# Performance work log

Hardware: AMD Instinct MI355X
Metric: run time of the kernel (lower is better)

## Reference

```python
import jax, jax.numpy as jnp
import numpy as np

B, N, E, T = 32768, 6, 6, 2  # batch graphs, nodes, edges (ring), edge types
H, DIN = 128, 3


def _ring_rel():
    # off_diag[i, (i+1)%N] = 1 -> edge e: sender i, receiver (i+1)%N
    send = np.arange(N)
    recv = (np.arange(N) + 1) % N
    eye = np.eye(N, dtype=np.float32)
    return jnp.asarray(eye[recv]), jnp.asarray(eye[send])  # rel_rec, rel_send [E,N]


def setup_inputs() -> dict:
    key = jax.random.key(0)
    ks = iter(jax.random.split(key, 40))
    rn = lambda shape, s=0.1: jax.random.normal(next(ks), shape, jnp.float32) * s
    rel_rec, rel_send = _ring_rel()
    inp = {
        'x': rn((B, N, DIN), 1.0),
        'rel_rec': rel_rec, 'rel_send': rel_send,
        'e1w1': rn((DIN, H)), 'e1b1': jnp.full((H,), 0.1), 'e1w2': rn((H, H)), 'e1b2': jnp.full((H,), 0.1),
        'e2w1': rn((2 * H, H)), 'e2b1': jnp.full((H,), 0.1), 'e2w2': rn((H, H)), 'e2b2': jnp.full((H,), 0.1),
        'e3w1': rn((H, H)), 'e3b1': jnp.full((H,), 0.1), 'e3w2': rn((H, H)), 'e3b2': jnp.full((H,), 0.1),
        'e4w1': rn((2 * H, H)), 'e4b1': jnp.full((H,), 0.1), 'e4w2': rn((H, H)), 'e4b2': jnp.full((H,), 0.1),
        'ew_out': rn((H, T)), 'eb_out': jnp.full((T,), 0.1),
        'd_msg_w1': rn((T, 2 * DIN, H)), 'd_msg_b1': rn((T, H), 0.01),
        'd_msg_w2': rn((T, H, H)), 'd_msg_b2': rn((T, H), 0.01),
        'd_out_w1': rn((DIN + H, H)), 'd_out_b1': rn((H,), 0.01),
        'd_out_w2': rn((H, H)), 'd_out_b2': rn((H,), 0.01),
        'd_out_w3': rn((H, DIN)), 'd_out_b3': rn((DIN,), 0.01),
    }
    return inp


def _mlp(h, w1, b1, w2, b2):
    # two-layer ELU MLP (dropout inactive at eval)
    return jax.nn.elu(jax.nn.elu(h @ w1 + b1) @ w2 + b2)


def reference(x, rel_rec, rel_send,
              e1w1, e1b1, e1w2, e1b2, e2w1, e2b1, e2w2, e2b2,
              e3w1, e3b1, e3w2, e3b2, e4w1, e4b1, e4w2, e4b2,
              ew_out, eb_out,
              d_msg_w1, d_msg_b1, d_msg_w2, d_msg_b2,
              d_out_w1, d_out_b1, d_out_w2, d_out_b2, d_out_w3, d_out_b3):
    node2edge = lambda h: jnp.concatenate(
        [jnp.einsum('en,bnh->beh', rel_rec, h), jnp.einsum('en,bnh->beh', rel_send, h)], axis=-1)

    # ---- GraphEncoder (factor=False) ----
    h = _mlp(x, e1w1, e1b1, e1w2, e1b2)                      # [B,N,H]
    he = _mlp(node2edge(h), e2w1, e2b1, e2w2, e2b2)          # [B,E,H]
    h2 = _mlp(he, e3w1, e3b1, e3w2, e3b2)                    # [B,E,H]
    h3 = _mlp(jnp.concatenate([h2, he], -1), e4w1, e4b1, e4w2, e4b2)
    logits = h3 @ ew_out + eb_out                            # [B,E,T]
    rel_type = jax.nn.softmax(logits, axis=-1)               # edge-type weights

    # ---- GraphDecoder single step (skip_first=False) ----
    recv = jnp.einsum('en,bnd->bed', rel_rec, x)             # [B,E,DIN]
    send = jnp.einsum('en,bnd->bed', rel_send, x)
    pre_msg = jnp.concatenate([recv, send], axis=-1)         # [B,E,2*DIN]
    # batched per-edge-type MLP: one grouped GEMM instead of a python loop of layers
    m = jax.nn.relu(jnp.einsum('bei,tih->bteh', pre_msg, d_msg_w1) + d_msg_b1[None, :, None, :])
    m = jax.nn.relu(jnp.einsum('bteh,tho->bteo', m, d_msg_w2) + d_msg_b2[None, :, None, :])
    all_msgs = jnp.einsum('bteh,bet->beh', m, rel_type)      # weight + accumulate over types
    agg_msgs = jnp.einsum('beh,en->bnh', all_msgs, rel_rec)  # edge -> node aggregation

    aug = jnp.concatenate([x, agg_msgs], axis=-1)            # [B,N,DIN+H]
    p = jax.nn.relu(aug @ d_out_w1 + d_out_b1)
    p = jax.nn.relu(p @ d_out_w2 + d_out_b2)
    p = p @ d_out_w3 + d_out_b3
    return x + p                                             # [B,N,DIN]
```

## Files before the change

### kernel.cpp

```cpp
#include <hip/hip_runtime.h>
#include <hip/hip_bf16.h>

typedef __bf16 bf16x8 __attribute__((ext_vector_type(8)));
typedef float floatx4 __attribute__((ext_vector_type(4)));

#define LDW 136
#define PXW 40

#define O_E1W2  0
#define O_E2W1  16384
#define O_E2W2  49152
#define O_E3W1  65536
#define O_E3W2  81920
#define O_E4W1  98304
#define O_E4W2  131072
#define O_DM2T0 147456
#define O_DM2T1 163840
#define O_DO1   180224
#define O_DO2   196608
#define O_EWOUT 212992
#define O_DW3   215040
#define O_E1W1P 217088
#define O_M1T0P 221184
#define O_M1T1P 225280
#define O_DO1XP 229376
#define WS_ELEMS 233472

__global__ void prep_kernel(const float* e1w2, const float* e2w1, const float* e2w2,
    const float* e3w1, const float* e3w2, const float* e4w1, const float* e4w2,
    const float* dmsg2, const float* dout1, const float* dout2,
    const float* ew_out, const float* dout_w3, const float* e1w1,
    const float* dmsg_w1, __hip_bfloat16* ws) {
  int idx = blockIdx.x * 256 + threadIdx.x;
  if (idx >= WS_ELEMS) return;
  float v;
  if (idx < O_E2W1)      { int l = idx;           v = e1w2[(l & 127) * 128 + (l >> 7)]; }
  else if (idx < O_E2W2) { int l = idx - O_E2W1;  v = e2w1[(l & 255) * 128 + (l >> 8)]; }
  else if (idx < O_E3W1) { int l = idx - O_E2W2;  v = e2w2[(l & 127) * 128 + (l >> 7)]; }
  else if (idx < O_E3W2) { int l = idx - O_E3W1;  v = e3w1[(l & 127) * 128 + (l >> 7)]; }
  else if (idx < O_E4W1) { int l = idx - O_E3W2;  v = e3w2[(l & 127) * 128 + (l >> 7)]; }
  else if (idx < O_E4W2) { int l = idx - O_E4W1;  v = e4w1[(l & 255) * 128 + (l >> 8)]; }
  else if (idx < O_DM2T0){ int l = idx - O_E4W2;  v = e4w2[(l & 127) * 128 + (l >> 7)]; }
  else if (idx < O_DM2T1){ int l = idx - O_DM2T0; v = dmsg2[(l & 127) * 128 + (l >> 7)]; }
  else if (idx < O_DO1)  { int l = idx - O_DM2T1; v = dmsg2[16384 + (l & 127) * 128 + (l >> 7)]; }
  else if (idx < O_DO2)  { int l = idx - O_DO1;   v = dout1[384 + (l & 127) * 128 + (l >> 7)]; }
  else if (idx < O_EWOUT){ int l = idx - O_DO2;   v = dout2[(l & 127) * 128 + (l >> 7)]; }
  else if (idx < O_DW3)  { int l = idx - O_EWOUT; int n = l >> 7;
                           v = (n < 2) ? ew_out[(l & 127) * 2 + n] : 0.f; }
  else if (idx < O_E1W1P){ int l = idx - O_DW3;   int n = l >> 7;
                           v = (n < 3) ? dout_w3[(l & 127) * 3 + n] : 0.f; }
  else if (idx < O_M1T0P){ int l = idx - O_E1W1P; int n = l >> 5, c = l & 31;
                           v = (c >= 3 && c < 6) ? e1w1[(c - 3) * 128 + n] : 0.f; }
  else if (idx < O_M1T1P){ int l = idx - O_M1T0P; int n = l >> 5, c = l & 31;
                           v = (c < 6) ? dmsg_w1[c * 128 + n] : 0.f; }
  else if (idx < O_DO1XP){ int l = idx - O_M1T1P; int n = l >> 5, c = l & 31;
                           v = (c < 6) ? dmsg_w1[768 + c * 128 + n] : 0.f; }
  else                   { int l = idx - O_DO1XP; int n = l >> 5, c = l & 31;
                           v = (c >= 3 && c < 6) ? dout1[(c - 3) * 128 + n] : 0.f; }
  ws[idx] = __float2bfloat16(v);
}

struct W4 { bf16x8 b[4]; };
struct W8 { bf16x8 b[8]; };

__global__ __launch_bounds__(512, 4) void nri_fused(
    const float* __restrict__ x,
    const float* __restrict__ e1b1, const float* __restrict__ e1b2,
    const float* __restrict__ e2b1, const float* __restrict__ e2b2,
    const float* __restrict__ e3b1, const float* __restrict__ e3b2,
    const float* __restrict__ e4b1, const float* __restrict__ e4b2,
    const float* __restrict__ eb_out,
    const float* __restrict__ dmsg_b1, const float* __restrict__ dmsg_b2,
    const float* __restrict__ dout_b1, const float* __restrict__ dout_b2,
    const float* __restrict__ dout_b3,
    const __bf16* __restrict__ wt, float* __restrict__ out)
{
  const int tid  = threadIdx.x;
  const int wave = tid >> 6;
  const int lane = tid & 63;
  const int nl   = lane & 15;
  const int quad = lane >> 4;
  const int colb = wave * 16 + nl;
  const int gx   = blockIdx.x * 288;

  __shared__ __align__(16) __hip_bfloat16 bufA[96 * LDW];
  __shared__ __align__(16) __hip_bfloat16 bufB[96 * LDW];
  __shared__ __align__(16) __hip_bfloat16 pxb[96 * PXW];
  __shared__ __align__(16) float biasL[16 * 128];
  __shared__ float rtw[192];
  __shared__ float xs[288];
  __shared__ float obuf[288];

  for (int i = tid; i < 288; i += 512) xs[i] = x[gx + i];
  for (int i = tid; i < 2048; i += 512) {
    int row = i >> 7, c = i & 127;
    float v;
    switch (row) {
      case 0: v = e1b1[c]; break;   case 1: v = e1b2[c]; break;
      case 2: v = e2b1[c]; break;   case 3: v = e2b2[c]; break;
      case 4: v = e3b1[c]; break;   case 5: v = e3b2[c]; break;
      case 6: v = e4b1[c]; break;   case 7: v = e4b2[c]; break;
      case 8: v = dmsg_b1[c]; break;  case 9: v = dmsg_b1[128 + c]; break;
      case 10: v = dmsg_b2[c]; break; case 11: v = dmsg_b2[128 + c]; break;
      case 12: v = dout_b1[c]; break; case 13: v = dout_b2[c]; break;
      case 14: v = (c < 2) ? eb_out[c] : 0.f; break;
      default: v = (c < 3) ? dout_b3[c] : 0.f; break;
    }
    biasL[i] = v;
  }
  for (int i = tid; i < 96 * 32; i += 512) {
    int row = i >> 5, c = i & 31;
    int e = row % 6;
    float v = 0.f;
    if (c < 3)      { int rr = row + ((e == 5) ? -5 : 1); v = x[gx + rr * 3 + c]; }
    else if (c < 6) v = x[gx + row * 3 + (c - 3)];
    pxb[row * PXW + c] = __float2bfloat16(v);
  }
  __syncthreads();

  auto initb = [&](floatx4 (&a)[6], int brow) {
    float bv = biasL[brow * 128 + colb];
    floatx4 v = {bv, bv, bv, bv};
#pragma unroll
    for (int mt = 0; mt < 6; ++mt) a[mt] = v;
  };

  auto loadW128 = [&](int wofs) {
    W4 w;
    const __bf16* p = wt + wofs + colb * 128 + quad * 8;
#pragma unroll
    for (int ks = 0; ks < 4; ++ks) w.b[ks] = *(const bf16x8*)(p + ks * 32);
    return w;
  };
  auto loadW256 = [&](int wofs) {
    W8 w;
    const __bf16* p = wt + wofs + colb * 256 + quad * 8;
#pragma unroll
    for (int ks = 0; ks < 8; ++ks) w.b[ks] = *(const bf16x8*)(p + ks * 32);
    return w;
  };
  auto loadW256half = [&](int wofs, int kh) {
    W4 w;
    const __bf16* p = wt + wofs + colb * 256 + kh * 128 + quad * 8;
#pragma unroll
    for (int ks = 0; ks < 4; ++ks) w.b[ks] = *(const bf16x8*)(p + ks * 32);
    return w;
  };

  auto gemmP = [&](floatx4 (&acc)[6], const W4& w, const __hip_bfloat16* in) {
    const __bf16* ab = (const __bf16*)(const void*)in;
#pragma unroll
    for (int ks = 0; ks < 4; ++ks) {
      int kk = ks * 32 + quad * 8;
#pragma unroll
      for (int mt = 0; mt < 6; ++mt) {
        bf16x8 a = *(const bf16x8*)(ab + (mt * 16 + nl) * LDW + kk);
        acc[mt] = __builtin_amdgcn_mfma_f32_16x16x32_bf16(a, w.b[ks], acc[mt], 0, 0, 0);
      }
    }
  };
  auto gemmP2 = [&](floatx4 (&accA)[6], const W4& wA, floatx4 (&accB)[6],
                    const W4& wB, const __hip_bfloat16* in) {
    const __bf16* ab = (const __bf16*)(const void*)in;
#pragma unroll
    for (int ks = 0; ks < 4; ++ks) {
      int kk = ks * 32 + quad * 8;
#pragma unroll
      for (int mt = 0; mt < 6; ++mt) {
        bf16x8 a = *(const bf16x8*)(ab + (mt * 16 + nl) * LDW + kk);
        accA[mt] = __builtin_amdgcn_mfma_f32_16x16x32_bf16(a, wA.b[ks], accA[mt], 0, 0, 0);
        accB[mt] = __builtin_amdgcn_mfma_f32_16x16x32_bf16(a, wB.b[ks], accB[mt], 0, 0, 0);
      }
    }
  };
  auto gemm256P = [&](floatx4 (&acc)[6], const W8& w, const __hip_bfloat16* in) {
    int rofs0[6], rofs1[6];
#pragma unroll
    for (int mt = 0; mt < 6; ++mt) {
      int r = mt * 16 + nl;
      rofs1[mt] = r * LDW;
      int e = r % 6;
      rofs0[mt] = (r + ((e == 5) ? -5 : 1)) * LDW;
    }
    const __bf16* ab = (const __bf16*)(const void*)in;
#pragma unroll
    for (int ks = 0; ks < 8; ++ks) {
      int kk = (ks & 3) * 32 + quad * 8;
      const int* rofs = (ks < 4) ? rofs0 : rofs1;
#pragma unroll
      for (int mt = 0; mt < 6; ++mt) {
        bf16x8 a = *(const bf16x8*)(ab + rofs[mt] + kk);
        acc[mt] = __builtin_amdgcn_mfma_f32_16x16x32_bf16(a, w.b[ks], acc[mt], 0, 0, 0);
      }
    }
  };
  auto gemm32 = [&](floatx4 (&acc)[6], int wofs) {
    const __bf16* pb = (const __bf16*)(const void*)pxb;
    bf16x8 b0 = *(const bf16x8*)(wt + wofs + colb * 32 + quad * 8);
#pragma unroll
    for (int mt = 0; mt < 6; ++mt) {
      bf16x8 a = *(const bf16x8*)(pb + (mt * 16 + nl) * PXW + quad * 8);
      acc[mt] = __builtin_amdgcn_mfma_f32_16x16x32_bf16(a, b0, acc[mt], 0, 0, 0);
    }
  };
  auto store_act = [&](floatx4 (&acc)[6], int act, __hip_bfloat16* ob) {
#pragma unroll
    for (int mt = 0; mt < 6; ++mt)
#pragma unroll
      for (int r = 0; r < 4; ++r) {
        float z = acc[mt][r];
        if (act == 1) z = (z > 0.f) ? z : (__expf(z) - 1.f);
        else z = fmaxf(z, 0.f);
        ob[(mt * 16 + quad * 4 + r) * LDW + colb] = __float2bfloat16(z);
      }
  };

  floatx4 acc[6], acc2[6];

  initb(acc, 0); gemm32(acc, O_E1W1P);
  W4 w2 = loadW128(O_E1W2);
  store_act(acc, 1, bufA);
  __syncthreads();
  initb(acc, 1); gemmP(acc, w2, bufA);
  W8 w3 = loadW256(O_E2W1);
  store_act(acc, 1, bufB);
  __syncthreads();
  initb(acc, 2); gemm256P(acc, w3, bufB);
  W4 w4 = loadW128(O_E2W2);
  store_act(acc, 1, bufA);
  __syncthreads();
  initb(acc, 3); gemmP(acc, w4, bufA);
  W4 w5 = loadW128(O_E3W1);
  W4 w5b = loadW256half(O_E4W1, 1);
  store_act(acc, 1, bufB);
  __syncthreads();
  initb(acc, 4); initb(acc2, 6);
  gemmP2(acc, w5, acc2, w5b, bufB);
  W4 w6 = loadW128(O_E3W2);
  store_act(acc, 1, bufA);
  __syncthreads();
  initb(acc, 5); gemmP(acc, w6, bufA);
  W4 w7 = loadW256half(O_E4W1, 0);
  store_act(acc, 1, bufB);
  __syncthreads();
  gemmP(acc2, w7, bufB);
  W4 w8 = loadW128(O_E4W2);
  store_act(acc2, 1, bufA);
  __syncthreads();
  initb(acc, 7); gemmP(acc, w8, bufA);
  store_act(acc, 1, bufB);
  __syncthreads();

  if (wave < 6) {
    int tile = wave;
    float bv = biasL[14 * 128 + nl];
    floatx4 lg = {bv, bv, bv, bv};
    const __bf16* ab = (const __bf16*)(const void*)bufB;
    const __bf16* wp = wt + O_EWOUT + nl * 128 + quad * 8;
#pragma unroll
    for (int ks = 0; ks < 4; ++ks) {
      bf16x8 a = *(const bf16x8*)(ab + (tile * 16 + nl) * LDW + ks * 32 + quad * 8);
      bf16x8 b = *(const bf16x8*)(wp + ks * 32);
      lg = __builtin_amdgcn_mfma_f32_16x16x32_bf16(a, b, lg, 0, 0, 0);
    }
    if (nl < 2) {
#pragma unroll
      for (int r = 0; r < 4; ++r)
        rtw[(tile * 16 + quad * 4 + r) * 2 + nl] = lg[r];
    }
  }
  __syncthreads();

  if (tid < 96) {
    float l0 = rtw[tid * 2], l1 = rtw[tid * 2 + 1];
    float mx = fmaxf(l0, l1);
    float ea = __expf(l0 - mx), eb = __expf(l1 - mx);
    float inv = 1.f / (ea + eb);
    rtw[tid * 2] = ea * inv; rtw[tid * 2 + 1] = eb * inv;
  }
  initb(acc, 8);  gemm32(acc, O_M1T0P);  store_act(acc, 2, bufA);
  initb(acc2, 9); gemm32(acc2, O_M1T1P); store_act(acc2, 2, bufB);
  W4 wm0 = loadW128(O_DM2T0);
  W4 wm1 = loadW128(O_DM2T1);
  __syncthreads();

  initb(acc, 10);  gemmP(acc, wm0, bufA);
  initb(acc2, 11); gemmP(acc2, wm1, bufB);
#pragma unroll
  for (int mt = 0; mt < 6; ++mt)
#pragma unroll
    for (int r = 0; r < 4; ++r) {
      int row = mt * 16 + quad * 4 + r;
      float r0 = rtw[row * 2], r1 = rtw[row * 2 + 1];
      acc[mt][r] = r0 * fmaxf(acc[mt][r], 0.f) + r1 * fmaxf(acc2[mt][r], 0.f);
    }
  W4 wd1 = loadW128(O_DO1);
  __syncthreads();

#pragma unroll
  for (int mt = 0; mt < 6; ++mt)
#pragma unroll
    for (int r = 0; r < 4; ++r) {
      int row = mt * 16 + quad * 4 + r;
      int e = row % 6;
      int orow = row + ((e == 5) ? -5 : 1);
      bufA[orow * LDW + colb] = __float2bfloat16(acc[mt][r]);
    }
  __syncthreads();

  initb(acc, 12); gemmP(acc, wd1, bufA); gemm32(acc, O_DO1XP);
  W4 wd2 = loadW128(O_DO2);
  store_act(acc, 2, bufB);
  __syncthreads();
  initb(acc, 13); gemmP(acc, wd2, bufB);
  store_act(acc, 2, bufA);
  __syncthreads();

  if (wave < 6) {
    int tile = wave;
    float bv = biasL[15 * 128 + nl];
    floatx4 d = {bv, bv, bv, bv};
    const __bf16* ab = (const __bf16*)(const void*)bufA;
    const __bf16* wp = wt + O_DW3 + nl * 128 + quad * 8;
#pragma unroll
    for (int ks = 0; ks < 4; ++ks) {
      bf16x8 a = *(const bf16x8*)(ab + (tile * 16 + nl) * LDW + ks * 32 + quad * 8);
      bf16x8 b = *(const bf16x8*)(wp + ks * 32);
      d = __builtin_amdgcn_mfma_f32_16x16x32_bf16(a, b, d, 0, 0, 0);
    }
    if (nl < 3) {
#pragma unroll
      for (int r = 0; r < 4; ++r) {
        int row = tile * 16 + quad * 4 + r;
        obuf[row * 3 + nl] = xs[row * 3 + nl] + d[r];
      }
    }
  }
  __syncthreads();
  for (int i = tid; i < 288; i += 512) out[gx + i] = obuf[i];
}

extern "C" void kernel_launch(void* const* d_in, const int* in_sizes, int n_in,
                              void* d_out, int out_size, void* d_ws, size_t ws_size,
                              hipStream_t stream) {
  const float* x       = (const float*)d_in[0];
  const float* e1w1    = (const float*)d_in[3];
  const float* e1b1    = (const float*)d_in[4];
  const float* e1w2    = (const float*)d_in[5];
  const float* e1b2    = (const float*)d_in[6];
  const float* e2w1    = (const float*)d_in[7];
  const float* e2b1    = (const float*)d_in[8];
  const float* e2w2    = (const float*)d_in[9];
  const float* e2b2    = (const float*)d_in[10];
  const float* e3w1    = (const float*)d_in[11];
  const float* e3b1    = (const float*)d_in[12];
  const float* e3w2    = (const float*)d_in[13];
  const float* e3b2    = (const float*)d_in[14];
  const float* e4w1    = (const float*)d_in[15];
  const float* e4b1    = (const float*)d_in[16];
  const float* e4w2    = (const float*)d_in[17];
  const float* e4b2    = (const float*)d_in[18];
  const float* ew_out  = (const float*)d_in[19];
  const float* eb_out  = (const float*)d_in[20];
  const float* dmsg_w1 = (const float*)d_in[21];
  const float* dmsg_b1 = (const float*)d_in[22];
  const float* dmsg_w2 = (const float*)d_in[23];
  const float* dmsg_b2 = (const float*)d_in[24];
  const float* dout_w1 = (const float*)d_in[25];
  const float* dout_b1 = (const float*)d_in[26];
  const float* dout_w2 = (const float*)d_in[27];
  const float* dout_b2 = (const float*)d_in[28];
  const float* dout_w3 = (const float*)d_in[29];
  const float* dout_b3 = (const float*)d_in[30];

  prep_kernel<<<(WS_ELEMS + 255) / 256, 256, 0, stream>>>(
      e1w2, e2w1, e2w2, e3w1, e3w2, e4w1, e4w2, dmsg_w2, dout_w1, dout_w2,
      ew_out, dout_w3, e1w1, dmsg_w1, (__hip_bfloat16*)d_ws);

  nri_fused<<<32768 / 16, 512, 0, stream>>>(
      x, e1b1, e1b2, e2b1, e2b2, e3b1, e3b2, e4b1, e4b2, eb_out,
      dmsg_b1, dmsg_b2, dout_b1, dout_b2, dout_b3,
      (const __bf16*)d_ws, (float*)d_out);
}
```

Before: 267.1 us.

## Shrink LDS footprint and raise occupancy by loading biases straight to registers

Removes the shared-memory bias table, the x staging buffer and the output staging buffer. Biases and the small K=32 weight fragments are now prefetched from global memory into registers just ahead of each layer. The padded input buffer shrinks from 40 to 8 columns, and only quad 0 loads A, with the other lanes feeding zeros. Launch bounds move from 4 to 6 blocks per SM to use the freed LDS for occupancy, at the cost of tighter register limits that may cause spills. Output is written directly from the final MFMA lanes rather than through a coalesced staging pass.

```diff
diff --git a/kernel.cpp b/kernel.cpp
--- a/kernel.cpp
+++ b/kernel.cpp
@@ -5,7 +5,7 @@
 typedef float floatx4 __attribute__((ext_vector_type(4)));
 
 #define LDW 136
-#define PXW 40
+#define PXW 8
 
 #define O_E1W2  0
 #define O_E2W1  16384
@@ -63,7 +63,7 @@
 struct W4 { bf16x8 b[4]; };
 struct W8 { bf16x8 b[8]; };
 
-__global__ __launch_bounds__(512, 4) void nri_fused(
+__global__ __launch_bounds__(512, 6) void nri_fused(
     const float* __restrict__ x,
     const float* __restrict__ e1b1, const float* __restrict__ e1b2,
     const float* __restrict__ e2b1, const float* __restrict__ e2b2,
@@ -86,40 +86,22 @@
   __shared__ __align__(16) __hip_bfloat16 bufA[96 * LDW];
   __shared__ __align__(16) __hip_bfloat16 bufB[96 * LDW];
   __shared__ __align__(16) __hip_bfloat16 pxb[96 * PXW];
-  __shared__ __align__(16) float biasL[16 * 128];
   __shared__ float rtw[192];
-  __shared__ float xs[288];
-  __shared__ float obuf[288];
-
-  for (int i = tid; i < 288; i += 512) xs[i] = x[gx + i];
-  for (int i = tid; i < 2048; i += 512) {
-    int row = i >> 7, c = i & 127;
-    float v;
-    switch (row) {
-      case 0: v = e1b1[c]; break;   case 1: v = e1b2[c]; break;
-      case 2: v = e2b1[c]; break;   case 3: v = e2b2[c]; break;
-      case 4: v = e3b1[c]; break;   case 5: v = e3b2[c]; break;
-      case 6: v = e4b1[c]; break;   case 7: v = e4b2[c]; break;
-      case 8: v = dmsg_b1[c]; break;  case 9: v = dmsg_b1[128 + c]; break;
-      case 10: v = dmsg_b2[c]; break; case 11: v = dmsg_b2[128 + c]; break;
-      case 12: v = dout_b1[c]; break; case 13: v = dout_b2[c]; break;
-      case 14: v = (c < 2) ? eb_out[c] : 0.f; break;
-      default: v = (c < 3) ? dout_b3[c] : 0.f; break;
-    }
-    biasL[i] = v;
-  }
-  for (int i = tid; i < 96 * 32; i += 512) {
-    int row = i >> 5, c = i & 31;
+
+  float b_s1 = e1b1[colb];
+  bf16x8 wk_s1 = *(const bf16x8*)(wt + O_E1W1P + colb * 32 + quad * 8);
+
+  for (int i = tid; i < 96 * PXW; i += 512) {
+    int row = i >> 3, c = i & 7;
     int e = row % 6;
     float v = 0.f;
     if (c < 3)      { int rr = row + ((e == 5) ? -5 : 1); v = x[gx + rr * 3 + c]; }
     else if (c < 6) v = x[gx + row * 3 + (c - 3)];
-    pxb[row * PXW + c] = __float2bfloat16(v);
+    pxb[i] = __float2bfloat16(v);
   }
   __syncthreads();
 
-  auto initb = [&](floatx4 (&a)[6], int brow) {
-    float bv = biasL[brow * 128 + colb];
+  auto initv = [&](floatx4 (&a)[6], float bv) {
     floatx4 v = {bv, bv, bv, bv};
 #pragma unroll
     for (int mt = 0; mt < 6; ++mt) a[mt] = v;
@@ -194,13 +176,13 @@
       }
     }
   };
-  auto gemm32 = [&](floatx4 (&acc)[6], int wofs) {
+  auto gemm32 = [&](floatx4 (&acc)[6], bf16x8 wfrag) {
     const __bf16* pb = (const __bf16*)(const void*)pxb;
-    bf16x8 b0 = *(const bf16x8*)(wt + wofs + colb * 32 + quad * 8);
 #pragma unroll
     for (int mt = 0; mt < 6; ++mt) {
-      bf16x8 a = *(const bf16x8*)(pb + (mt * 16 + nl) * PXW + quad * 8);
-      acc[mt] = __builtin_amdgcn_mfma_f32_16x16x32_bf16(a, b0, acc[mt], 0, 0, 0);
+      bf16x8 a = {0, 0, 0, 0, 0, 0, 0, 0};
+      if (quad == 0) a = *(const bf16x8*)(pb + (mt * 16 + nl) * PXW);
+      acc[mt] = __builtin_amdgcn_mfma_f32_16x16x32_bf16(a, wfrag, acc[mt], 0, 0, 0);
     }
   };
   auto store_act = [&](floatx4 (&acc)[6], int act, __hip_bfloat16* ob) {
@@ -217,44 +199,55 @@
 
   floatx4 acc[6], acc2[6];
 
-  initb(acc, 0); gemm32(acc, O_E1W1P);
+  initv(acc, b_s1); gemm32(acc, wk_s1);
   W4 w2 = loadW128(O_E1W2);
+  float b_s2 = e1b2[colb];
   store_act(acc, 1, bufA);
   __syncthreads();
-  initb(acc, 1); gemmP(acc, w2, bufA);
+  initv(acc, b_s2); gemmP(acc, w2, bufA);
   W8 w3 = loadW256(O_E2W1);
+  float b_s3 = e2b1[colb];
   store_act(acc, 1, bufB);
   __syncthreads();
-  initb(acc, 2); gemm256P(acc, w3, bufB);
+  initv(acc, b_s3); gemm256P(acc, w3, bufB);
   W4 w4 = loadW128(O_E2W2);
+  float b_s4 = e2b2[colb];
   store_act(acc, 1, bufA);
   __syncthreads();
-  initb(acc, 3); gemmP(acc, w4, bufA);
+  initv(acc, b_s4); gemmP(acc, w4, bufA);
   W4 w5 = loadW128(O_E3W1);
   W4 w5b = loadW256half(O_E4W1, 1);
+  float b_s5 = e3b1[colb];
+  float b2_s5 = e4b1[colb];
   store_act(acc, 1, bufB);
   __syncthreads();
-  initb(acc, 4); initb(acc2, 6);
+  initv(acc, b_s5); initv(acc2, b2_s5);
   gemmP2(acc, w5, acc2, w5b, bufB);
   W4 w6 = loadW128(O_E3W2);
+  float b_s6 = e3b2[colb];
   store_act(acc, 1, bufA);
   __syncthreads();
-  initb(acc, 5); gemmP(acc, w6, bufA);
+  initv(acc, b_s6); gemmP(acc, w6, bufA);
   W4 w7 = loadW256half(O_E4W1, 0);
   store_act(acc, 1, bufB);
   __syncthreads();
   gemmP(acc2, w7, bufB);
   W4 w8 = loadW128(O_E4W2);
+  float b_s8 = e4b2[colb];
   store_act(acc2, 1, bufA);
   __syncthreads();
-  initb(acc, 7); gemmP(acc, w8, bufA);
+  initv(acc, b_s8); gemmP(acc, w8, bufA);
+  float ebv = (nl < 2) ? eb_out[nl] : 0.f;
+  bf16x8 wk10a = *(const bf16x8*)(wt + O_M1T0P + colb * 32 + quad * 8);
+  bf16x8 wk10b = *(const bf16x8*)(wt + O_M1T1P + colb * 32 + quad * 8);
+  float b_m0 = dmsg_b1[colb];
+  float b_m1 = dmsg_b1[128 + colb];
   store_act(acc, 1, bufB);
   __syncthreads();
 
   if (wave < 6) {
     int tile = wave;
-    float bv = biasL[14 * 128 + nl];
-    floatx4 lg = {bv, bv, bv, bv};
+    floatx4 lg = {ebv, ebv, ebv, ebv};
     const __bf16* ab = (const __bf16*)(const void*)bufB;
     const __bf16* wp = wt + O_EWOUT + nl * 128 + quad * 8;
 #pragma unroll
@@ -278,14 +271,16 @@
     float inv = 1.f / (ea + eb);
     rtw[tid * 2] = ea * inv; rtw[tid * 2 + 1] = eb * inv;
   }
-  initb(acc, 8);  gemm32(acc, O_M1T0P);  store_act(acc, 2, bufA);
-  initb(acc2, 9); gemm32(acc2, O_M1T1P); store_act(acc2, 2, bufB);
+  initv(acc, b_m0);  gemm32(acc, wk10a);  store_act(acc, 2, bufA);
+  initv(acc2, b_m1); gemm32(acc2, wk10b); store_act(acc2, 2, bufB);
   W4 wm0 = loadW128(O_DM2T0);
   W4 wm1 = loadW128(O_DM2T1);
-  __syncthreads();
-
-  initb(acc, 10);  gemmP(acc, wm0, bufA);
-  initb(acc2, 11); gemmP(acc2, wm1, bufB);
+  float b_d0 = dmsg_b2[colb];
+  float b_d1 = dmsg_b2[128 + colb];
+  __syncthreads();
+
+  initv(acc, b_d0);  gemmP(acc, wm0, bufA);
+  initv(acc2, b_d1); gemmP(acc2, wm1, bufB);
 #pragma unroll
   for (int mt = 0; mt < 6; ++mt)
 #pragma unroll
@@ -295,6 +290,8 @@
       acc[mt][r] = r0 * fmaxf(acc[mt][r], 0.f) + r1 * fmaxf(acc2[mt][r], 0.f);
     }
   W4 wd1 = loadW128(O_DO1);
+  bf16x8 wk13 = *(const bf16x8*)(wt + O_DO1XP + colb * 32 + quad * 8);
+  float b_p1 = dout_b1[colb];
   __syncthreads();
 
 #pragma unroll
@@ -308,18 +305,19 @@
     }
   __syncthreads();
 
-  initb(acc, 12); gemmP(acc, wd1, bufA); gemm32(acc, O_DO1XP);
+  initv(acc, b_p1); gemmP(acc, wd1, bufA); gemm32(acc, wk13);
   W4 wd2 = loadW128(O_DO2);
+  float b_p2 = dout_b2[colb];
   store_act(acc, 2, bufB);
   __syncthreads();
-  initb(acc, 13); gemmP(acc, wd2, bufB);
+  initv(acc, b_p2); gemmP(acc, wd2, bufB);
+  float b3v = (nl < 3) ? dout_b3[nl] : 0.f;
   store_act(acc, 2, bufA);
   __syncthreads();
 
   if (wave < 6) {
     int tile = wave;
-    float bv = biasL[15 * 128 + nl];
-    floatx4 d = {bv, bv, bv, bv};
+    floatx4 d = {b3v, b3v, b3v, b3v};
     const __bf16* ab = (const __bf16*)(const void*)bufA;
     const __bf16* wp = wt + O_DW3 + nl * 128 + quad * 8;
 #pragma unroll
@@ -332,12 +330,10 @@
 #pragma unroll
       for (int r = 0; r < 4; ++r) {
         int row = tile * 16 + quad * 4 + r;
-        obuf[row * 3 + nl] = xs[row * 3 + nl] + d[r];
+        out[gx + row * 3 + nl] = x[gx + row * 3 + nl] + d[r];
       }
     }
   }
-  __syncthreads();
-  for (int i = tid; i < 288; i += 512) out[gx + i] = obuf[i];
 }
 
 extern "C" void kernel_launch(void* const* d_in, const int* in_sizes, int n_in,
```

Result: slower. 317.9 us (+19.0%).
